# Kernel tuning notes

Measured on AMD Instinct MI355X. Metric: run time of the kernel, lower is better.

## Reference

```python
import jax, jax.numpy as jnp
import numpy as np

NUM_EXPERTS = 64
TOP_K = 8
HIDDEN = 2048
INTER = 768


def setup_inputs() -> dict:
    key = jax.random.key(0)
    k1, k2, k3, k4, k5 = jax.random.split(key, 5)
    hidden_states = jax.random.normal(k1, (4, 256, HIDDEN), dtype=jnp.float32)
    # router gate: Linear(hidden, num_experts, bias=False); stored as [H, E]
    gate_w = jax.random.normal(k2, (HIDDEN, NUM_EXPERTS), dtype=jnp.float32) * 0.02
    # per-expert SwiGLU FFN weights (w13 split into gate/up, plus down)
    w_gate = jax.random.normal(k3, (NUM_EXPERTS, HIDDEN, INTER), dtype=jnp.float32) * 0.02
    w_up = jax.random.normal(k4, (NUM_EXPERTS, HIDDEN, INTER), dtype=jnp.float32) * 0.02
    w_down = jax.random.normal(k5, (NUM_EXPERTS, INTER, HIDDEN), dtype=jnp.float32) * 0.02
    return {"hidden_states": hidden_states, "gate_w": gate_w,
            "w_gate": w_gate, "w_up": w_up, "w_down": w_down}


def reference(hidden_states, gate_w, w_gate, w_up, w_down):
    orig_shape = hidden_states.shape
    x = hidden_states.reshape(-1, orig_shape[-1])          # [T, H]
    T = x.shape[0]
    # router: softmax over expert logits, top-k select, renormalize (norm_topk_prob=True)
    router_logits = x @ gate_w                              # [T, E]
    probs = jax.nn.softmax(router_logits.astype(jnp.float32), axis=-1)
    top_vals, top_idx = jax.lax.top_k(probs, TOP_K)         # [T, K]
    top_vals = top_vals / jnp.sum(top_vals, axis=-1, keepdims=True)
    # dense [T, E] routing-weight matrix (zeros off the top-k) — jit-friendly dispatch
    rw = jnp.zeros((T, NUM_EXPERTS), dtype=x.dtype)
    rw = rw.at[jnp.arange(T)[:, None], top_idx].set(top_vals)
    # SwiGLU expert FFN evaluated per (token, expert), weighted-combined
    g = jnp.einsum('th,ehi->tei', x, w_gate)                # [T, E, I]
    u = jnp.einsum('th,ehi->tei', x, w_up)                  # [T, E, I]
    h = jax.nn.silu(g) * u                                  # [T, E, I]
    h = h * rw[:, :, None]                                  # fold routing weight before down-proj
    out = jnp.einsum('tei,eih->th', h, w_down)              # [T, H]
    return out.reshape(orig_shape)
```

## Files before the change

### kernel.cpp

```cpp
#include <hip/hip_runtime.h>
#include <cstdint>

#define T_TOK 1024
#define HID   2048
#define NEXP  64
#define TOPK  8
#define INTER 768

typedef __attribute__((ext_vector_type(8))) short short8;
typedef __attribute__((ext_vector_type(4))) float f32x4;

__device__ __forceinline__ unsigned short f2bf(float f){
  unsigned u = __float_as_uint(f);
  u += 0x7FFFu + ((u >> 16) & 1u);
  return (unsigned short)(u >> 16);
}

__global__ void k_convert_x(const float* __restrict__ x, unsigned short* __restrict__ xbf){
  int gid = blockIdx.x * 256 + threadIdx.x;
  const float4* src = (const float4*)(x + (size_t)gid * 8);
  float4 a = src[0], b = src[1];
  uint4 p;
  p.x = f2bf(a.x) | ((unsigned)f2bf(a.y) << 16);
  p.y = f2bf(a.z) | ((unsigned)f2bf(a.w) << 16);
  p.z = f2bf(b.x) | ((unsigned)f2bf(b.y) << 16);
  p.w = f2bf(b.z) | ((unsigned)f2bf(b.w) << 16);
  *(uint4*)(xbf + (size_t)gid * 8) = p;
}

__global__ void k_router(const float* __restrict__ x, const float* __restrict__ gw,
                         int* __restrict__ top_idx, float* __restrict__ top_w){
  int t = blockIdx.x;
  int tid = threadIdx.x;
  __shared__ float  xs[HID];
  __shared__ double part[4][NEXP];
  for (int i = tid; i < HID; i += 256) xs[i] = x[(size_t)t * HID + i];
  __syncthreads();
  int e = tid & 63, q = tid >> 6;
  double acc = 0.0;
  const float* gp = gw + e;
  #pragma unroll 8
  for (int h = q * 512; h < q * 512 + 512; ++h)
    acc += (double)xs[h] * (double)gp[(size_t)h * NEXP];
  part[q][e] = acc;
  __syncthreads();
  if (tid < 64){
    float logit = (float)(part[0][e] + part[1][e] + part[2][e] + part[3][e]);
    float cur = logit;
    float vals[TOPK]; int idxs[TOPK];
    #pragma unroll
    for (int k = 0; k < TOPK; ++k){
      float m = cur; int mi = e;
      #pragma unroll
      for (int off = 32; off > 0; off >>= 1){
        float ov = __shfl_xor(m, off);
        int   oi = __shfl_xor(mi, off);
        if (ov > m || (ov == m && oi < mi)){ m = ov; mi = oi; }
      }
      vals[k] = m; idxs[k] = mi;
      if (e == mi) cur = -1e30f;
    }
    float mx = vals[0], s = 0.f, ev[TOPK];
    #pragma unroll
    for (int k = 0; k < TOPK; ++k){ ev[k] = expf(vals[k] - mx); s += ev[k]; }
    #pragma unroll
    for (int k = 0; k < TOPK; ++k)
      if (e == k){ top_idx[t * TOPK + k] = idxs[k]; top_w[t * TOPK + k] = ev[k] / s; }
  }
}

__global__ void k_hist(const int* __restrict__ top_idx, int* __restrict__ offs){
  __shared__ int hist[NEXP];
  int tid = threadIdx.x;
  if (tid < NEXP) hist[tid] = 0;
  __syncthreads();
  for (int j = tid; j < T_TOK * TOPK; j += 256) atomicAdd(&hist[top_idx[j]], 1);
  __syncthreads();
  if (tid == 0){
    int run = 0;
    for (int e = 0; e < NEXP; ++e){ offs[e] = run; run += hist[e]; }
    offs[NEXP] = run;
  }
}

__global__ void k_compact(const int* __restrict__ top_idx, const float* __restrict__ top_w,
                          const int* __restrict__ offs, int* __restrict__ list_t,
                          float* __restrict__ list_w, int* __restrict__ slot_of){
  int e = blockIdx.x, tid = threadIdx.x;
  __shared__ int sc[256];
  int j0 = tid * 32, cnt = 0;
  for (int jj = 0; jj < 32; ++jj) cnt += (top_idx[j0 + jj] == e);
  sc[tid] = cnt; __syncthreads();
  for (int d = 1; d < 256; d <<= 1){
    int v = (tid >= d) ? sc[tid - d] : 0;
    __syncthreads();
    sc[tid] += v;
    __syncthreads();
  }
  int pos = offs[e] + sc[tid] - cnt;
  for (int jj = 0; jj < 32; ++jj){
    int j = j0 + jj;
    if (top_idx[j] == e){
      list_t[pos]  = j >> 3;
      list_w[pos]  = top_w[j];
      slot_of[j]   = pos;
      ++pos;
    }
  }
}

#define BARRIER() do { asm volatile("s_waitcnt lgkmcnt(0)" ::: "memory"); \
                       __builtin_amdgcn_s_barrier(); } while (0)

__global__ __launch_bounds__(256) void k_gateup(
    const unsigned short* __restrict__ xbf, const float* __restrict__ wg,
    const float* __restrict__ wu, const int* __restrict__ offs,
    const int* __restrict__ list_t, const float* __restrict__ list_w,
    unsigned short* __restrict__ act){
  int e  = blockIdx.y;
  int i0 = blockIdx.x * 32;
  int beg = offs[e], n_e = offs[e + 1] - beg;
  if (n_e <= 0) return;
  int tid = threadIdx.x, lane = tid & 63, wid = tid >> 6;
  int cLane = lane & 15, kqB = (lane >> 4) << 4;

  __shared__ unsigned short lB[2][2][32 * 64];
  __shared__ int   sTok[192];
  __shared__ float sWgt[192];
  char* ldsBase = (char*)&lB[0][0][0];

  int colB = tid & 31, kg = tid >> 5;
  int wOff = (kg << 4) ^ ((colB & 7) << 4);
  const float* gBase = wg + (size_t)e * HID * INTER + i0 + colB;
  const float* uBase = wu + (size_t)e * HID * INTER + i0 + colB;

#define GU_ISSUE_B(T, rg_, ru_) { \
    const float* _gp = gBase + (size_t)((T) * 64 + kg * 8) * INTER; \
    const float* _up = uBase + (size_t)((T) * 64 + kg * 8) * INTER; \
    _Pragma("unroll") for (int j = 0; j < 8; ++j){ \
      rg_[j] = _gp[(size_t)j * INTER]; ru_[j] = _up[(size_t)j * INTER]; } }

#define GU_WRITE_B(BUF, rg_, ru_) { \
    uint4 _p; \
    _p.x = f2bf(rg_[0]) | ((unsigned)f2bf(rg_[1]) << 16); \
    _p.y = f2bf(rg_[2]) | ((unsigned)f2bf(rg_[3]) << 16); \
    _p.z = f2bf(rg_[4]) | ((unsigned)f2bf(rg_[5]) << 16); \
    _p.w = f2bf(rg_[6]) | ((unsigned)f2bf(rg_[7]) << 16); \
    *(uint4*)(ldsBase + (BUF) * 8192 + colB * 128 + wOff) = _p; \
    _p.x = f2bf(ru_[0]) | ((unsigned)f2bf(ru_[1]) << 16); \
    _p.y = f2bf(ru_[2]) | ((unsigned)f2bf(ru_[3]) << 16); \
    _p.z = f2bf(ru_[4]) | ((unsigned)f2bf(ru_[5]) << 16); \
    _p.w = f2bf(ru_[6]) | ((unsigned)f2bf(ru_[7]) << 16); \
    *(uint4*)(ldsBase + (BUF) * 8192 + 4096 + colB * 128 + wOff) = _p; }

#define GU_ISSUE_A(T, ra_) { \
    int _kk = (T) * 64 + ((lane >> 4) << 3); \
    _Pragma("unroll") for (int mf = 0; mf < 3; ++mf){ \
      const unsigned short* _ap = xbf + (size_t)tokA[mf] * HID + _kk; \
      ra_[mf][0] = *(const short8*)_ap; \
      ra_[mf][1] = *(const short8*)(_ap + 32); } }

#define GU_MFMA(BUF, ra_) { \
    _Pragma("unroll") for (int ks = 0; ks < 2; ++ks){ \
      short8 _bg[2], _bu[2]; \
      _Pragma("unroll") for (int nf = 0; nf < 2; ++nf){ \
        int _col = nf * 16 + cLane; \
        int _kb = (ks * 64 + kqB) ^ ((_col & 7) << 4); \
        _bg[nf] = *(const short8*)(ldsBase + (BUF) * 8192 + _col * 128 + _kb); \
        _bu[nf] = *(const short8*)(ldsBase + (BUF) * 8192 + 4096 + _col * 128 + _kb); } \
      _Pragma("unroll") for (int mf = 0; mf < 3; ++mf) \
        _Pragma("unroll") for (int nf = 0; nf < 2; ++nf){ \
          accg[mf][nf] = __builtin_amdgcn_mfma_f32_16x16x32_bf16(ra_[mf][ks], _bg[nf], accg[mf][nf], 0, 0, 0); \
          accu[mf][nf] = __builtin_amdgcn_mfma_f32_16x16x32_bf16(ra_[mf][ks], _bu[nf], accu[mf][nf], 0, 0, 0); } } }

  for (int m0 = 0; m0 < n_e; m0 += 192){
    __syncthreads();
    if (tid < 192){
      int sl = beg + m0 + tid;
      if (m0 + tid < n_e){ sTok[tid] = list_t[sl]; sWgt[tid] = list_w[sl]; }
      else               { sTok[tid] = list_t[beg]; sWgt[tid] = 0.f; }
    }
    __syncthreads();
    int tokA[3];
    #pragma unroll
    for (int mf = 0; mf < 3; ++mf) tokA[mf] = sTok[wid * 48 + mf * 16 + cLane];

    float sg0[8], su0[8], sg1[8], su1[8];
    short8 rA[3][2];
    f32x4 accg[3][2] = {}; f32x4 accu[3][2] = {};

    GU_ISSUE_B(0, sg0, su0);
    GU_ISSUE_B(1, sg1, su1);
    GU_WRITE_B(0, sg0, su0);
    BARRIER();
    #pragma unroll 1
    for (int t = 0; t < 32; t += 2){
      GU_ISSUE_A(t, rA);
      if (t + 2 < 32) GU_ISSUE_B(t + 2, sg0, su0);
      GU_MFMA(0, rA);
      GU_WRITE_B(1, sg1, su1);
      BARRIER();
      GU_ISSUE_A(t + 1, rA);
      if (t + 3 < 32) GU_ISSUE_B(t + 3, sg1, su1);
      GU_MFMA(1, rA);
      if (t + 2 < 32) GU_WRITE_B(0, sg0, su0);
      BARRIER();
    }

    #pragma unroll
    for (int mf = 0; mf < 3; ++mf){
      #pragma unroll
      for (int rr = 0; rr < 4; ++rr){
        int r = wid * 48 + mf * 16 + ((lane >> 4) << 2) + rr;
        if (m0 + r < n_e){
          int slot = beg + m0 + r;
          float wgt = sWgt[r];
          #pragma unroll
          for (int nf = 0; nf < 2; ++nf){
            float g = accg[mf][nf][rr], u = accu[mf][nf][rr];
            float h = (g / (1.f + expf(-g))) * u * wgt;
            act[(size_t)slot * INTER + i0 + nf * 16 + cLane] = f2bf(h);
          }
        }
      }
    }
  }
}

__global__ __launch_bounds__(256) void k_down(
    const unsigned short* __restrict__ act, const float* __restrict__ wd,
    const int* __restrict__ offs, const int* __restrict__ list_t,
    float* __restrict__ contrib, float* __restrict__ out, int atomicMode){
  int e  = blockIdx.y;
  int n0 = blockIdx.x * 64;
  int beg = offs[e], n_e = offs[e + 1] - beg;
  if (n_e <= 0) return;
  int tid = threadIdx.x, lane = tid & 63, wid = tid >> 6;
  int cLane = lane & 15, kqB = (lane >> 4) << 4;

  __shared__ unsigned short lB[2][64 * 64];
  __shared__ int sTok[192];
  char* ldsBase = (char*)&lB[0][0];

  int colB = tid & 63, kg = tid >> 6;
  int wOff0 = ((kg << 5) + 0)  ^ ((colB & 7) << 4);
  int wOff1 = ((kg << 5) + 16) ^ ((colB & 7) << 4);
  const float* dBase = wd + (size_t)e * INTER * HID + n0 + colB;

#define DN_ISSUE_B(T, rb_) { \
    const float* _p = dBase + (size_t)((T) * 64 + kg * 16) * HID; \
    _Pragma("unroll") for (int j = 0; j < 16; ++j) rb_[j] = _p[(size_t)j * HID]; }

#define DN_WRITE_B(BUF, rb_) { \
    uint4 _p; \
    _p.x = f2bf(rb_[0]) | ((unsigned)f2bf(rb_[1]) << 16); \
    _p.y = f2bf(rb_[2]) | ((unsigned)f2bf(rb_[3]) << 16); \
    _p.z = f2bf(rb_[4]) | ((unsigned)f2bf(rb_[5]) << 16); \
    _p.w = f2bf(rb_[6]) | ((unsigned)f2bf(rb_[7]) << 16); \
    *(uint4*)(ldsBase + (BUF) * 8192 + colB * 128 + wOff0) = _p; \
    _p.x = f2bf(rb_[8])  | ((unsigned)f2bf(rb_[9])  << 16); \
    _p.y = f2bf(rb_[10]) | ((unsigned)f2bf(rb_[11]) << 16); \
    _p.z = f2bf(rb_[12]) | ((unsigned)f2bf(rb_[13]) << 16); \
    _p.w = f2bf(rb_[14]) | ((unsigned)f2bf(rb_[15]) << 16); \
    *(uint4*)(ldsBase + (BUF) * 8192 + colB * 128 + wOff1) = _p; }

#define DN_ISSUE_A(T, ra_) { \
    int _kk = (T) * 64 + ((lane >> 4) << 3); \
    _Pragma("unroll") for (int mf = 0; mf < 3; ++mf){ \
      const unsigned short* _ap = act + (size_t)aslot[mf] * INTER + _kk; \
      ra_[mf][0] = *(const short8*)_ap; \
      ra_[mf][1] = *(const short8*)(_ap + 32); } }

#define DN_MFMA(BUF, ra_) { \
    _Pragma("unroll") for (int ks = 0; ks < 2; ++ks){ \
      short8 _bf[4]; \
      _Pragma("unroll") for (int nf = 0; nf < 4; ++nf){ \
        int _col = nf * 16 + cLane; \
        int _kb = (ks * 64 + kqB) ^ ((_col & 7) << 4); \
        _bf[nf] = *(const short8*)(ldsBase + (BUF) * 8192 + _col * 128 + _kb); } \
      _Pragma("unroll") for (int mf = 0; mf < 3; ++mf) \
        _Pragma("unroll") for (int nf = 0; nf < 4; ++nf) \
          acc[mf][nf] = __builtin_amdgcn_mfma_f32_16x16x32_bf16(ra_[mf][ks], _bf[nf], acc[mf][nf], 0, 0, 0); } }

  for (int m0 = 0; m0 < n_e; m0 += 192){
    __syncthreads();
    if (tid < 192){
      int sl = beg + m0 + tid;
      sTok[tid] = (m0 + tid < n_e) ? list_t[sl] : 0;
    }
    __syncthreads();
    int aslot[3];
    #pragma unroll
    for (int mf = 0; mf < 3; ++mf){
      int r = wid * 48 + mf * 16 + cLane;
      aslot[mf] = (m0 + r < n_e) ? (beg + m0 + r) : beg;
    }
    float s0[16], s1[16];
    short8 rA[3][2];
    f32x4 acc[3][4] = {};

    DN_ISSUE_B(0, s0);
    DN_ISSUE_B(1, s1);
    DN_WRITE_B(0, s0);
    BARRIER();
    #pragma unroll 1
    for (int t = 0; t < 12; t += 2){
      DN_ISSUE_A(t, rA);
      if (t + 2 < 12) DN_ISSUE_B(t + 2, s0);
      DN_MFMA(0, rA);
      DN_WRITE_B(1, s1);
      BARRIER();
      DN_ISSUE_A(t + 1, rA);
      if (t + 3 < 12) DN_ISSUE_B(t + 3, s1);
      DN_MFMA(1, rA);
      if (t + 2 < 12) DN_WRITE_B(0, s0);
      BARRIER();
    }

    #pragma unroll
    for (int mf = 0; mf < 3; ++mf){
      #pragma unroll
      for (int rr = 0; rr < 4; ++rr){
        int r = wid * 48 + mf * 16 + ((lane >> 4) << 2) + rr;
        if (m0 + r < n_e){
          int slot = beg + m0 + r;
          #pragma unroll
          for (int nf = 0; nf < 4; ++nf){
            float v = acc[mf][nf][rr];
            int h = n0 + nf * 16 + cLane;
            if (atomicMode) atomicAdd(&out[(size_t)sTok[r] * HID + h], v);
            else            contrib[(size_t)slot * HID + h] = v;
          }
        }
      }
    }
  }
}

__global__ void k_reduce(const float* __restrict__ contrib, const int* __restrict__ slot_of,
                         float* __restrict__ out){
  int bx = blockIdx.x;
  int t = bx >> 1, seg = bx & 1, tid = threadIdx.x;
  __shared__ int ss[TOPK];
  if (tid < TOPK) ss[tid] = slot_of[t * TOPK + tid];
  __syncthreads();
  int h = (seg * 256 + tid) * 4;
  f32x4 s = {0.f, 0.f, 0.f, 0.f};
  #pragma unroll
  for (int k = 0; k < TOPK; ++k){
    f32x4 v = *(const f32x4*)(contrib + (size_t)ss[k] * HID + h);
    s += v;
  }
  *(f32x4*)(out + (size_t)t * HID + h) = s;
}

extern "C" void kernel_launch(void* const* d_in, const int* in_sizes, int n_in,
                              void* d_out, int out_size, void* d_ws, size_t ws_size,
                              hipStream_t stream){
  const float* x   = (const float*)d_in[0];
  const float* gw  = (const float*)d_in[1];
  const float* wgp = (const float*)d_in[2];
  const float* wup = (const float*)d_in[3];
  const float* wdp = (const float*)d_in[4];
  float* out = (float*)d_out;
  char* ws = (char*)d_ws;

  int*   top_idx = (int*)  (ws + 0);
  float* top_w   = (float*)(ws + 32768);
  int*   offs    = (int*)  (ws + 65536);
  int*   list_t  = (int*)  (ws + 69632);
  float* list_w  = (float*)(ws + 102400);
  int*   slot_of = (int*)  (ws + 135168);
  unsigned short* xbf = (unsigned short*)(ws + 167936);
  unsigned short* act = (unsigned short*)(ws + 167936 + 4194304);
  float* contrib = (float*)(ws + 167936 + 4194304 + 12582912);
  size_t need_full = (size_t)167936 + 4194304 + 12582912 + 67108864;
  int atomicMode = (ws_size < need_full) ? 1 : 0;

  k_convert_x<<<1024, 256, 0, stream>>>(x, xbf);
  k_router   <<<1024, 256, 0, stream>>>(x, gw, top_idx, top_w);
  k_hist     <<<1,    256, 0, stream>>>(top_idx, offs);
  k_compact  <<<64,   256, 0, stream>>>(top_idx, top_w, offs, list_t, list_w, slot_of);
  k_gateup   <<<dim3(INTER / 32, NEXP), 256, 0, stream>>>(xbf, wgp, wup, offs, list_t, list_w, act);
  if (atomicMode){
    hipMemsetAsync(d_out, 0, (size_t)out_size * sizeof(float), stream);
    k_down  <<<dim3(HID / 64, NEXP), 256, 0, stream>>>(act, wdp, offs, list_t, contrib, out, 1);
  } else {
    k_down  <<<dim3(HID / 64, NEXP), 256, 0, stream>>>(act, wdp, offs, list_t, contrib, out, 0);
    k_reduce<<<2048, 256, 0, stream>>>(contrib, slot_of, out);
  }
}
```

Baseline: 421.1 us.

## Coalesce expert weight loads and use LDS transpose reads for MFMA B fragments

Weight tiles are now loaded as row-contiguous float4 vectors instead of strided scalar column loads, stored k-major in LDS, and read back with ds_read_b64_tr_b16 transposing reads to form MFMA B fragments. The column tile per block is halved in both the gate/up and down kernels, which doubles the grid. A-operand loads are restructured to match the transposed K ordering and are prefetched one step ahead into a second register buffer. The aim is to cut uncoalesced global traffic on the fp32 weights. In exchange, each block gets less reuse of its activation rows, and the explicit waits after the transpose reads may serialize LDS reads with MFMA work.

```diff
diff --git a/kernel.cpp b/kernel.cpp
--- a/kernel.cpp
+++ b/kernel.cpp
@@ -9,12 +9,32 @@
 
 typedef __attribute__((ext_vector_type(8))) short short8;
 typedef __attribute__((ext_vector_type(4))) float f32x4;
+typedef __attribute__((ext_vector_type(2))) unsigned int uint2v;
 
 __device__ __forceinline__ unsigned short f2bf(float f){
   unsigned u = __float_as_uint(f);
   u += 0x7FFFu + ((u >> 16) & 1u);
   return (unsigned short)(u >> 16);
 }
+
+#define LDSA(p) ((unsigned)(uintptr_t)(__attribute__((address_space(3))) void*)(p))
+
+__device__ __forceinline__ uint2v tr0(unsigned a){
+  uint2v r; asm volatile("ds_read_b64_tr_b16 %0, %1" : "=v"(r) : "v"(a)); return r;
+}
+__device__ __forceinline__ uint2v tr512(unsigned a){
+  uint2v r; asm volatile("ds_read_b64_tr_b16 %0, %1 offset:512" : "=v"(r) : "v"(a)); return r;
+}
+__device__ __forceinline__ short8 mkfrag(uint2v lo, uint2v hi){
+  union { unsigned u[4]; short8 s; } v;
+  v.u[0] = lo[0]; v.u[1] = lo[1]; v.u[2] = hi[0]; v.u[3] = hi[1];
+  return v.s;
+}
+
+#define TRWAIT() do { asm volatile("s_waitcnt lgkmcnt(0)" ::: "memory"); \
+                      __builtin_amdgcn_sched_barrier(0); } while (0)
+#define BARRIER() do { asm volatile("s_waitcnt lgkmcnt(0)" ::: "memory"); \
+                       __builtin_amdgcn_s_barrier(); } while (0)
 
 __global__ void k_convert_x(const float* __restrict__ x, unsigned short* __restrict__ xbf){
   int gid = blockIdx.x * 256 + threadIdx.x;
@@ -109,69 +129,59 @@
   }
 }
 
-#define BARRIER() do { asm volatile("s_waitcnt lgkmcnt(0)" ::: "memory"); \
-                       __builtin_amdgcn_s_barrier(); } while (0)
-
 __global__ __launch_bounds__(256) void k_gateup(
     const unsigned short* __restrict__ xbf, const float* __restrict__ wg,
     const float* __restrict__ wu, const int* __restrict__ offs,
     const int* __restrict__ list_t, const float* __restrict__ list_w,
     unsigned short* __restrict__ act){
+  const int KT = 32;
   int e  = blockIdx.y;
-  int i0 = blockIdx.x * 32;
+  int i0 = blockIdx.x * 16;
   int beg = offs[e], n_e = offs[e + 1] - beg;
   if (n_e <= 0) return;
   int tid = threadIdx.x, lane = tid & 63, wid = tid >> 6;
-  int cLane = lane & 15, kqB = (lane >> 4) << 4;
-
-  __shared__ unsigned short lB[2][2][32 * 64];
+  int cL = lane & 15, qL = lane >> 4;
+
+  __shared__ unsigned short lB[2][2][64 * 16];
   __shared__ int   sTok[192];
   __shared__ float sWgt[192];
-  char* ldsBase = (char*)&lB[0][0][0];
-
-  int colB = tid & 31, kg = tid >> 5;
-  int wOff = (kg << 4) ^ ((colB & 7) << 4);
-  const float* gBase = wg + (size_t)e * HID * INTER + i0 + colB;
-  const float* uBase = wu + (size_t)e * HID * INTER + i0 + colB;
-
-#define GU_ISSUE_B(T, rg_, ru_) { \
-    const float* _gp = gBase + (size_t)((T) * 64 + kg * 8) * INTER; \
-    const float* _up = uBase + (size_t)((T) * 64 + kg * 8) * INTER; \
-    _Pragma("unroll") for (int j = 0; j < 8; ++j){ \
-      rg_[j] = _gp[(size_t)j * INTER]; ru_[j] = _up[(size_t)j * INTER]; } }
-
-#define GU_WRITE_B(BUF, rg_, ru_) { \
-    uint4 _p; \
-    _p.x = f2bf(rg_[0]) | ((unsigned)f2bf(rg_[1]) << 16); \
-    _p.y = f2bf(rg_[2]) | ((unsigned)f2bf(rg_[3]) << 16); \
-    _p.z = f2bf(rg_[4]) | ((unsigned)f2bf(rg_[5]) << 16); \
-    _p.w = f2bf(rg_[6]) | ((unsigned)f2bf(rg_[7]) << 16); \
-    *(uint4*)(ldsBase + (BUF) * 8192 + colB * 128 + wOff) = _p; \
-    _p.x = f2bf(ru_[0]) | ((unsigned)f2bf(ru_[1]) << 16); \
-    _p.y = f2bf(ru_[2]) | ((unsigned)f2bf(ru_[3]) << 16); \
-    _p.z = f2bf(ru_[4]) | ((unsigned)f2bf(ru_[5]) << 16); \
-    _p.w = f2bf(ru_[6]) | ((unsigned)f2bf(ru_[7]) << 16); \
-    *(uint4*)(ldsBase + (BUF) * 8192 + 4096 + colB * 128 + wOff) = _p; }
+
+  int bk = tid >> 2, bc = (tid & 3) * 4;
+  const float* gS = wg + ((size_t)e * HID + bk) * INTER + i0 + bc;
+  const float* uS = wu + ((size_t)e * HID + bk) * INTER + i0 + bc;
+  unsigned rAddr = LDSA(&lB[0][0][0]) + (unsigned)lane * 8;
+
+#define GU_ISSUE_B(T, bs_) { \
+    bs_[0] = *(const float4*)(gS + (size_t)(T) * 64 * INTER); \
+    bs_[1] = *(const float4*)(uS + (size_t)(T) * 64 * INTER); }
+
+#define GU_WRITE_B(BUF, bs_) { \
+    uint2v _p; \
+    _p[0] = f2bf(bs_[0].x) | ((unsigned)f2bf(bs_[0].y) << 16); \
+    _p[1] = f2bf(bs_[0].z) | ((unsigned)f2bf(bs_[0].w) << 16); \
+    *(uint2v*)&lB[BUF][0][bk * 16 + bc] = _p; \
+    _p[0] = f2bf(bs_[1].x) | ((unsigned)f2bf(bs_[1].y) << 16); \
+    _p[1] = f2bf(bs_[1].z) | ((unsigned)f2bf(bs_[1].w) << 16); \
+    *(uint2v*)&lB[BUF][1][bk * 16 + bc] = _p; }
 
 #define GU_ISSUE_A(T, ra_) { \
-    int _kk = (T) * 64 + ((lane >> 4) << 3); \
     _Pragma("unroll") for (int mf = 0; mf < 3; ++mf){ \
-      const unsigned short* _ap = xbf + (size_t)tokA[mf] * HID + _kk; \
-      ra_[mf][0] = *(const short8*)_ap; \
-      ra_[mf][1] = *(const short8*)(_ap + 32); } }
+      const unsigned short* _ap = xbf + (size_t)tokA[mf] * HID + (T) * 64 + 4 * qL; \
+      _Pragma("unroll") for (int ks = 0; ks < 2; ++ks){ \
+        uint2v _lo = *(const uint2v*)(_ap + ks * 32); \
+        uint2v _hi = *(const uint2v*)(_ap + ks * 32 + 16); \
+        ra_[mf][ks] = mkfrag(_lo, _hi); } } }
 
 #define GU_MFMA(BUF, ra_) { \
     _Pragma("unroll") for (int ks = 0; ks < 2; ++ks){ \
-      short8 _bg[2], _bu[2]; \
-      _Pragma("unroll") for (int nf = 0; nf < 2; ++nf){ \
-        int _col = nf * 16 + cLane; \
-        int _kb = (ks * 64 + kqB) ^ ((_col & 7) << 4); \
-        _bg[nf] = *(const short8*)(ldsBase + (BUF) * 8192 + _col * 128 + _kb); \
-        _bu[nf] = *(const short8*)(ldsBase + (BUF) * 8192 + 4096 + _col * 128 + _kb); } \
-      _Pragma("unroll") for (int mf = 0; mf < 3; ++mf) \
-        _Pragma("unroll") for (int nf = 0; nf < 2; ++nf){ \
-          accg[mf][nf] = __builtin_amdgcn_mfma_f32_16x16x32_bf16(ra_[mf][ks], _bg[nf], accg[mf][nf], 0, 0, 0); \
-          accu[mf][nf] = __builtin_amdgcn_mfma_f32_16x16x32_bf16(ra_[mf][ks], _bu[nf], accu[mf][nf], 0, 0, 0); } } }
+      unsigned _b = rAddr + (BUF) * 4096 + ks * 1024; \
+      uint2v _g1 = tr0(_b),        _g2 = tr512(_b); \
+      uint2v _u1 = tr0(_b + 2048), _u2 = tr512(_b + 2048); \
+      TRWAIT(); \
+      short8 _fg = mkfrag(_g1, _g2), _fu = mkfrag(_u1, _u2); \
+      _Pragma("unroll") for (int mf = 0; mf < 3; ++mf){ \
+        accg[mf] = __builtin_amdgcn_mfma_f32_16x16x32_bf16(ra_[mf][ks], _fg, accg[mf], 0, 0, 0); \
+        accu[mf] = __builtin_amdgcn_mfma_f32_16x16x32_bf16(ra_[mf][ks], _fu, accu[mf], 0, 0, 0); } } }
 
   for (int m0 = 0; m0 < n_e; m0 += 192){
     __syncthreads();
@@ -183,27 +193,29 @@
     __syncthreads();
     int tokA[3];
     #pragma unroll
-    for (int mf = 0; mf < 3; ++mf) tokA[mf] = sTok[wid * 48 + mf * 16 + cLane];
-
-    float sg0[8], su0[8], sg1[8], su1[8];
-    short8 rA[3][2];
-    f32x4 accg[3][2] = {}; f32x4 accu[3][2] = {};
-
-    GU_ISSUE_B(0, sg0, su0);
-    GU_ISSUE_B(1, sg1, su1);
-    GU_WRITE_B(0, sg0, su0);
+    for (int mf = 0; mf < 3; ++mf) tokA[mf] = sTok[wid * 48 + mf * 16 + cL];
+
+    float4 bs0[2], bs1[2];
+    short8 rA0[3][2], rA1[3][2];
+    f32x4 accg[3] = {}; f32x4 accu[3] = {};
+
+    GU_ISSUE_A(0, rA0);
+    GU_ISSUE_B(0, bs0);
+    GU_ISSUE_B(1, bs1);
+    GU_WRITE_B(0, bs0);
     BARRIER();
+
     #pragma unroll 1
-    for (int t = 0; t < 32; t += 2){
-      GU_ISSUE_A(t, rA);
-      if (t + 2 < 32) GU_ISSUE_B(t + 2, sg0, su0);
-      GU_MFMA(0, rA);
-      GU_WRITE_B(1, sg1, su1);
+    for (int t = 0; t < KT; t += 2){
+      if (t + 1 < KT) GU_ISSUE_A(t + 1, rA1);
+      if (t + 2 < KT) GU_ISSUE_B(t + 2, bs0);
+      GU_MFMA(0, rA0);
+      if (t + 1 < KT) GU_WRITE_B(1, bs1);
       BARRIER();
-      GU_ISSUE_A(t + 1, rA);
-      if (t + 3 < 32) GU_ISSUE_B(t + 3, sg1, su1);
-      GU_MFMA(1, rA);
-      if (t + 2 < 32) GU_WRITE_B(0, sg0, su0);
+      if (t + 2 < KT) GU_ISSUE_A(t + 2, rA0);
+      if (t + 3 < KT) GU_ISSUE_B(t + 3, bs1);
+      GU_MFMA(1, rA1);
+      if (t + 2 < KT) GU_WRITE_B(0, bs0);
       BARRIER();
     }
 
@@ -211,16 +223,13 @@
     for (int mf = 0; mf < 3; ++mf){
       #pragma unroll
       for (int rr = 0; rr < 4; ++rr){
-        int r = wid * 48 + mf * 16 + ((lane >> 4) << 2) + rr;
+        int r = wid * 48 + mf * 16 + qL * 4 + rr;
         if (m0 + r < n_e){
           int slot = beg + m0 + r;
           float wgt = sWgt[r];
-          #pragma unroll
-          for (int nf = 0; nf < 2; ++nf){
-            float g = accg[mf][nf][rr], u = accu[mf][nf][rr];
-            float h = (g / (1.f + expf(-g))) * u * wgt;
-            act[(size_t)slot * INTER + i0 + nf * 16 + cLane] = f2bf(h);
-          }
+          float g = accg[mf][rr], u = accu[mf][rr];
+          float h = (g / (1.f + expf(-g))) * u * wgt;
+          act[(size_t)slot * INTER + i0 + cL] = f2bf(h);
         }
       }
     }
@@ -231,56 +240,53 @@
     const unsigned short* __restrict__ act, const float* __restrict__ wd,
     const int* __restrict__ offs, const int* __restrict__ list_t,
     float* __restrict__ contrib, float* __restrict__ out, int atomicMode){
+  const int KT = 12;
   int e  = blockIdx.y;
-  int n0 = blockIdx.x * 64;
+  int n0 = blockIdx.x * 32;
   int beg = offs[e], n_e = offs[e + 1] - beg;
   if (n_e <= 0) return;
   int tid = threadIdx.x, lane = tid & 63, wid = tid >> 6;
-  int cLane = lane & 15, kqB = (lane >> 4) << 4;
-
-  __shared__ unsigned short lB[2][64 * 64];
+  int cL = lane & 15, qL = lane >> 4;
+
+  __shared__ unsigned short lB[2][2][64 * 16];
   __shared__ int sTok[192];
-  char* ldsBase = (char*)&lB[0][0];
-
-  int colB = tid & 63, kg = tid >> 6;
-  int wOff0 = ((kg << 5) + 0)  ^ ((colB & 7) << 4);
-  int wOff1 = ((kg << 5) + 16) ^ ((colB & 7) << 4);
-  const float* dBase = wd + (size_t)e * INTER * HID + n0 + colB;
-
-#define DN_ISSUE_B(T, rb_) { \
-    const float* _p = dBase + (size_t)((T) * 64 + kg * 16) * HID; \
-    _Pragma("unroll") for (int j = 0; j < 16; ++j) rb_[j] = _p[(size_t)j * HID]; }
-
-#define DN_WRITE_B(BUF, rb_) { \
-    uint4 _p; \
-    _p.x = f2bf(rb_[0]) | ((unsigned)f2bf(rb_[1]) << 16); \
-    _p.y = f2bf(rb_[2]) | ((unsigned)f2bf(rb_[3]) << 16); \
-    _p.z = f2bf(rb_[4]) | ((unsigned)f2bf(rb_[5]) << 16); \
-    _p.w = f2bf(rb_[6]) | ((unsigned)f2bf(rb_[7]) << 16); \
-    *(uint4*)(ldsBase + (BUF) * 8192 + colB * 128 + wOff0) = _p; \
-    _p.x = f2bf(rb_[8])  | ((unsigned)f2bf(rb_[9])  << 16); \
-    _p.y = f2bf(rb_[10]) | ((unsigned)f2bf(rb_[11]) << 16); \
-    _p.z = f2bf(rb_[12]) | ((unsigned)f2bf(rb_[13]) << 16); \
-    _p.w = f2bf(rb_[14]) | ((unsigned)f2bf(rb_[15]) << 16); \
-    *(uint4*)(ldsBase + (BUF) * 8192 + colB * 128 + wOff1) = _p; }
+
+  int bk = tid >> 3, bc = (tid & 7) * 4;
+  const float* dS = wd + ((size_t)e * INTER + bk) * HID + n0 + bc;
+  int wpan = bc >> 4, wcc = bc & 15;
+  unsigned rAddr = LDSA(&lB[0][0][0]) + (unsigned)lane * 8;
+
+#define DN_ISSUE_B(T, bs_) { \
+    bs_[0] = *(const float4*)(dS + (size_t)(T) * 64 * HID); \
+    bs_[1] = *(const float4*)(dS + (size_t)((T) * 64 + 32) * HID); }
+
+#define DN_WRITE_B(BUF, bs_) { \
+    uint2v _p; \
+    _p[0] = f2bf(bs_[0].x) | ((unsigned)f2bf(bs_[0].y) << 16); \
+    _p[1] = f2bf(bs_[0].z) | ((unsigned)f2bf(bs_[0].w) << 16); \
+    *(uint2v*)&lB[BUF][wpan][bk * 16 + wcc] = _p; \
+    _p[0] = f2bf(bs_[1].x) | ((unsigned)f2bf(bs_[1].y) << 16); \
+    _p[1] = f2bf(bs_[1].z) | ((unsigned)f2bf(bs_[1].w) << 16); \
+    *(uint2v*)&lB[BUF][wpan][(bk + 32) * 16 + wcc] = _p; }
 
 #define DN_ISSUE_A(T, ra_) { \
-    int _kk = (T) * 64 + ((lane >> 4) << 3); \
     _Pragma("unroll") for (int mf = 0; mf < 3; ++mf){ \
-      const unsigned short* _ap = act + (size_t)aslot[mf] * INTER + _kk; \
-      ra_[mf][0] = *(const short8*)_ap; \
-      ra_[mf][1] = *(const short8*)(_ap + 32); } }
+      const unsigned short* _ap = act + (size_t)aslot[mf] * INTER + (T) * 64 + 4 * qL; \
+      _Pragma("unroll") for (int ks = 0; ks < 2; ++ks){ \
+        uint2v _lo = *(const uint2v*)(_ap + ks * 32); \
+        uint2v _hi = *(const uint2v*)(_ap + ks * 32 + 16); \
+        ra_[mf][ks] = mkfrag(_lo, _hi); } } }
 
 #define DN_MFMA(BUF, ra_) { \
     _Pragma("unroll") for (int ks = 0; ks < 2; ++ks){ \
-      short8 _bf[4]; \
-      _Pragma("unroll") for (int nf = 0; nf < 4; ++nf){ \
-        int _col = nf * 16 + cLane; \
-        int _kb = (ks * 64 + kqB) ^ ((_col & 7) << 4); \
-        _bf[nf] = *(const short8*)(ldsBase + (BUF) * 8192 + _col * 128 + _kb); } \
-      _Pragma("unroll") for (int mf = 0; mf < 3; ++mf) \
-        _Pragma("unroll") for (int nf = 0; nf < 4; ++nf) \
-          acc[mf][nf] = __builtin_amdgcn_mfma_f32_16x16x32_bf16(ra_[mf][ks], _bf[nf], acc[mf][nf], 0, 0, 0); } }
+      unsigned _b = rAddr + (BUF) * 4096 + ks * 1024; \
+      uint2v _a1 = tr0(_b),        _a2 = tr512(_b); \
+      uint2v _b1 = tr0(_b + 2048), _b2 = tr512(_b + 2048); \
+      TRWAIT(); \
+      short8 _f0 = mkfrag(_a1, _a2), _f1 = mkfrag(_b1, _b2); \
+      _Pragma("unroll") for (int mf = 0; mf < 3; ++mf){ \
+        acc[mf][0] = __builtin_amdgcn_mfma_f32_16x16x32_bf16(ra_[mf][ks], _f0, acc[mf][0], 0, 0, 0); \
+        acc[mf][1] = __builtin_amdgcn_mfma_f32_16x16x32_bf16(ra_[mf][ks], _f1, acc[mf][1], 0, 0, 0); } } }
 
   for (int m0 = 0; m0 < n_e; m0 += 192){
     __syncthreads();
@@ -292,28 +298,30 @@
     int aslot[3];
     #pragma unroll
     for (int mf = 0; mf < 3; ++mf){
-      int r = wid * 48 + mf * 16 + cLane;
+      int r = wid * 48 + mf * 16 + cL;
       aslot[mf] = (m0 + r < n_e) ? (beg + m0 + r) : beg;
     }
-    float s0[16], s1[16];
-    short8 rA[3][2];
-    f32x4 acc[3][4] = {};
-
-    DN_ISSUE_B(0, s0);
-    DN_ISSUE_B(1, s1);
-    DN_WRITE_B(0, s0);
+    float4 bs0[2], bs1[2];
+    short8 rA0[3][2], rA1[3][2];
+    f32x4 acc[3][2] = {};
+
+    DN_ISSUE_A(0, rA0);
+    DN_ISSUE_B(0, bs0);
+    DN_ISSUE_B(1, bs1);
+    DN_WRITE_B(0, bs0);
     BARRIER();
+
     #pragma unroll 1
-    for (int t = 0; t < 12; t += 2){
-      DN_ISSUE_A(t, rA);
-      if (t + 2 < 12) DN_ISSUE_B(t + 2, s0);
-      DN_MFMA(0, rA);
-      DN_WRITE_B(1, s1);
+    for (int t = 0; t < KT; t += 2){
+      if (t + 1 < KT) DN_ISSUE_A(t + 1, rA1);
+      if (t + 2 < KT) DN_ISSUE_B(t + 2, bs0);
+      DN_MFMA(0, rA0);
+      if (t + 1 < KT) DN_WRITE_B(1, bs1);
       BARRIER();
-      DN_ISSUE_A(t + 1, rA);
-      if (t + 3 < 12) DN_ISSUE_B(t + 3, s1);
-      DN_MFMA(1, rA);
-      if (t + 2 < 12) DN_WRITE_B(0, s0);
+      if (t + 2 < KT) DN_ISSUE_A(t + 2, rA0);
+      if (t + 3 < KT) DN_ISSUE_B(t + 3, bs1);
+      DN_MFMA(1, rA1);
+      if (t + 2 < KT) DN_WRITE_B(0, bs0);
       BARRIER();
     }
 
@@ -321,13 +329,13 @@
     for (int mf = 0; mf < 3; ++mf){
       #pragma unroll
       for (int rr = 0; rr < 4; ++rr){
-        int r = wid * 48 + mf * 16 + ((lane >> 4) << 2) + rr;
+        int r = wid * 48 + mf * 16 + qL * 4 + rr;
         if (m0 + r < n_e){
           int slot = beg + m0 + r;
           #pragma unroll
-          for (int nf = 0; nf < 4; ++nf){
+          for (int nf = 0; nf < 2; ++nf){
             float v = acc[mf][nf][rr];
-            int h = n0 + nf * 16 + cLane;
+            int h = n0 + nf * 16 + cL;
             if (atomicMode) atomicAdd(&out[(size_t)sTok[r] * HID + h], v);
             else            contrib[(size_t)slot * HID + h] = v;
           }
@@ -381,12 +389,12 @@
   k_router   <<<1024, 256, 0, stream>>>(x, gw, top_idx, top_w);
   k_hist     <<<1,    256, 0, stream>>>(top_idx, offs);
   k_compact  <<<64,   256, 0, stream>>>(top_idx, top_w, offs, list_t, list_w, slot_of);
-  k_gateup   <<<dim3(INTER / 32, NEXP), 256, 0, stream>>>(xbf, wgp, wup, offs, list_t, list_w, act);
+  k_gateup   <<<dim3(INTER / 16, NEXP), 256, 0, stream>>>(xbf, wgp, wup, offs, list_t, list_w, act);
   if (atomicMode){
     hipMemsetAsync(d_out, 0, (size_t)out_size * sizeof(float), stream);
-    k_down  <<<dim3(HID / 64, NEXP), 256, 0, stream>>>(act, wdp, offs, list_t, contrib, out, 1);
+    k_down  <<<dim3(HID / 32, NEXP), 256, 0, stream>>>(act, wdp, offs, list_t, contrib, out, 1);
   } else {
-    k_down  <<<dim3(HID / 64, NEXP), 256, 0, stream>>>(act, wdp, offs, list_t, contrib, out, 0);
+    k_down  <<<dim3(HID / 32, NEXP), 256, 0, stream>>>(act, wdp, offs, list_t, contrib, out, 0);
     k_reduce<<<2048, 256, 0, stream>>>(contrib, slot_of, out);
   }
 }
```

After: 878.5 us. 109% more time.
